# Kernel optimization log

Hardware: AMD Instinct MI355X
Metric: run time of the kernel (lower is better)

## Reference

```python
import jax, jax.numpy as jnp
import numpy as np

N = 50000
E = 800000
F_IN = 500
H = 5          # heads
C = 32         # per-head channels
HID = H * C    # 160
NC = 20        # num_classes
G = 8          # number of graphs in batch
SLOPE_ATT = 0.2   # GATConv attention leaky slope (PyG default)
SLOPE_ACT = 0.01  # F.leaky_relu default


def _layernorm(x, scale, bias, eps=1e-5):
    mu = jnp.mean(x, axis=-1, keepdims=True)
    var = jnp.var(x, axis=-1, keepdims=True)
    return (x - mu) * jax.lax.rsqrt(var + eps) * scale + bias


def _edge_softmax(logits, dst, num_nodes):
    # segment softmax over incoming edges of each destination node
    m = jax.ops.segment_max(logits, dst, num_segments=num_nodes)
    ex = jnp.exp(logits - m[dst])
    s = jax.ops.segment_sum(ex, dst, num_segments=num_nodes)
    return ex / (s[dst] + 1e-16)


def _gat_layer(x, src, dst, W, a_src, a_dst, b):
    n = x.shape[0]
    h = (x @ W).reshape(n, H, C)                       # [N,H,C]
    al_s = jnp.einsum('nhc,hc->nh', h, a_src)          # [N,H]
    al_d = jnp.einsum('nhc,hc->nh', h, a_dst)
    logits = jax.nn.leaky_relu(al_s[src] + al_d[dst], SLOPE_ATT)  # [Et,H]
    alpha = _edge_softmax(logits, dst, n)              # [Et,H]
    msg = h[src] * alpha[..., None]                    # [Et,H,C]
    out = jax.ops.segment_sum(msg, dst, num_segments=n).reshape(n, HID) + b
    return out, alpha


def setup_inputs():
    key = jax.random.key(0)
    ks = jax.random.split(key, 24)
    p = lambda k, shp: jax.random.normal(k, shp, jnp.float32) * 0.05
    x = jax.random.normal(ks[0], (N, F_IN), jnp.float32)
    edge_index = jax.random.randint(ks[1], (2, E), 0, N, jnp.int64)
    batch = jnp.sort(jax.random.randint(ks[2], (N,), 0, G, jnp.int64))
    return {
        'x': x, 'edge_index': edge_index, 'batch': batch,
        'W1': p(ks[3], (F_IN, HID)), 'a_src1': p(ks[4], (H, C)), 'a_dst1': p(ks[5], (H, C)), 'b1': jnp.zeros((HID,), jnp.float32),
        'ln1_s': jnp.ones((HID,), jnp.float32), 'ln1_b': jnp.zeros((HID,), jnp.float32),
        'W2': p(ks[6], (HID, HID)), 'a_src2': p(ks[7], (H, C)), 'a_dst2': p(ks[8], (H, C)), 'b2': jnp.zeros((HID,), jnp.float32),
        'ln2_s': jnp.ones((HID,), jnp.float32), 'ln2_b': jnp.zeros((HID,), jnp.float32),
        'Wm': p(ks[9], (HID, HID)), 'bm': jnp.zeros((HID,), jnp.float32),
        'Wmlp1': p(ks[10], (HID, HID)), 'bmlp1': jnp.zeros((HID,), jnp.float32),
        'ln3_s': jnp.ones((HID,), jnp.float32), 'ln3_b': jnp.zeros((HID,), jnp.float32),
        'Wmlp2': p(ks[11], (HID, NC)), 'bmlp2': jnp.zeros((NC,), jnp.float32),
    }


def reference(x, edge_index, batch, W1, a_src1, a_dst1, b1, ln1_s, ln1_b,
              W2, a_src2, a_dst2, b2, ln2_s, ln2_b, Wm, bm,
              Wmlp1, bmlp1, ln3_s, ln3_b, Wmlp2, bmlp2):
    n = x.shape[0]
    # PyG GATConv adds self-loops by default
    loops = jnp.arange(n, dtype=edge_index.dtype)
    src = jnp.concatenate([edge_index[0], loops])
    dst = jnp.concatenate([edge_index[1], loops])

    h1, alpha1 = _gat_layer(x, src, dst, W1, a_src1, a_dst1, b1)
    h1 = jax.nn.leaky_relu(h1, SLOPE_ACT)
    h1 = _layernorm(h1, ln1_s, ln1_b)      # dropout = identity at eval

    h2, alpha2 = _gat_layer(h1, src, dst, W2, a_src2, a_dst2, b2)
    h2 = jax.nn.leaky_relu(h2, SLOPE_ACT)
    h2 = _layernorm(h2, ln2_s, ln2_b)

    xo = jax.nn.leaky_relu(h2 @ Wm + bm, SLOPE_ACT)   # [N,HID]

    # global_mean_pool over batch assignment
    sums = jax.ops.segment_sum(xo, batch, num_segments=G)
    cnts = jax.ops.segment_sum(jnp.ones((n, 1), xo.dtype), batch, num_segments=G)
    pooled = sums / jnp.maximum(cnts, 1.0)            # [G,HID]

    z = pooled @ Wmlp1 + bmlp1
    z = jax.nn.relu(_layernorm(z, ln3_s, ln3_b))
    rec = z @ Wmlp2 + bmlp2                           # [G,NC]
    return xo, rec, alpha1, alpha2
```

## Files before the change

kernel.cpp:

```cpp
#include <hip/hip_runtime.h>
#include <hip/hip_bf16.h>
#include <cstdint>
#include <cstddef>

#define NN   50000
#define EE   800000
#define ET_  (EE + NN)
#define FIN  500
#define HID_ 160
#define NC_  20
#define GG   8
#define GB1  ((NN + 63) / 64)
#define NK1  16
#define NK2  5

typedef __attribute__((ext_vector_type(8))) short ab8;
typedef __attribute__((ext_vector_type(4))) float f4;

static __device__ __forceinline__ unsigned short f2bf(float v) {
    union { float f; uint32_t u; } c; c.f = v;
    uint32_t r = c.u + 0x7FFFu + ((c.u >> 16) & 1u);
    return (unsigned short)(r >> 16);
}

static __device__ __forceinline__ float2 bf2f2(uint32_t u) {
    union { uint32_t u; float f; } a, b;
    a.u = u << 16;
    b.u = u & 0xffff0000u;
    return make_float2(a.f, b.f);
}

static __device__ __forceinline__ int lbound_i(const int* arr, int n, int val) {
    int lo = 0, hi = n;
    while (lo < hi) { int mid = (lo + hi) >> 1; if (arr[mid] < val) lo = mid + 1; else hi = mid; }
    return lo;
}

__global__ __launch_bounds__(256) void k_hist(const int* __restrict__ ei, int* __restrict__ deg) {
    int e = blockIdx.x * 256 + threadIdx.x;
    if (e >= ET_) return;
    int d = (e < EE) ? ei[EE + e] : (e - EE);
    atomicAdd(&deg[d], 1);
}

__global__ __launch_bounds__(256) void k_scan1(const int* __restrict__ deg, int* __restrict__ rowptr,
                                               int* __restrict__ bsum) {
    __shared__ int s[256];
    int t = threadIdx.x;
    int base = blockIdx.x * 1024 + t * 4;
    int v0 = (base + 0 < NN) ? deg[base + 0] : 0;
    int v1 = (base + 1 < NN) ? deg[base + 1] : 0;
    int v2 = (base + 2 < NN) ? deg[base + 2] : 0;
    int v3 = (base + 3 < NN) ? deg[base + 3] : 0;
    int tot = v0 + v1 + v2 + v3;
    s[t] = tot;
    __syncthreads();
    for (int off = 1; off < 256; off <<= 1) {
        int y = (t >= off) ? s[t - off] : 0;
        __syncthreads();
        s[t] += y;
        __syncthreads();
    }
    int excl = s[t] - tot;
    if (t == 255) bsum[blockIdx.x] = s[255];
    if (base + 0 < NN) rowptr[base + 0] = excl;  excl += v0;
    if (base + 1 < NN) rowptr[base + 1] = excl;  excl += v1;
    if (base + 2 < NN) rowptr[base + 2] = excl;  excl += v2;
    if (base + 3 < NN) rowptr[base + 3] = excl;
}

__global__ void k_scan2(int* __restrict__ bsum, int nb) {
    int t = threadIdx.x;
    int v = (t < nb) ? bsum[t] : 0;
    int orig = v;
    for (int off = 1; off < 64; off <<= 1) {
        int y = __shfl_up(v, off);
        if (t >= off) v += y;
    }
    if (t < nb) bsum[t] = v - orig;
}

__global__ __launch_bounds__(256) void k_scan3(int* __restrict__ rowptr, const int* __restrict__ bsum,
                                               int* __restrict__ cursor) {
    int i = blockIdx.x * 256 + threadIdx.x;
    if (i < NN) {
        int r = rowptr[i] + bsum[i >> 10];
        rowptr[i] = r;
        cursor[i] = r;
    }
    if (i == NN) rowptr[NN] = ET_;
}

__global__ __launch_bounds__(256) void k_scatter(const int* __restrict__ ei, int* __restrict__ cursor,
                                                 int* __restrict__ esrc) {
    int e = blockIdx.x * 256 + threadIdx.x;
    if (e >= ET_) return;
    int s, d;
    if (e < EE) { s = ei[e]; d = ei[EE + e]; } else { s = e - EE; d = e - EE; }
    int slot = atomicAdd(&cursor[d], 1);
    esrc[slot] = s;
}

__global__ __launch_bounds__(256) void k_prep_all(const float* __restrict__ W1, ab8* __restrict__ B1,
                                                  const float* __restrict__ W2, ab8* __restrict__ B2,
                                                  const float* __restrict__ Wm, ab8* __restrict__ Bm,
                                                  float* __restrict__ pooled) {
    int idx = blockIdx.x * 256 + threadIdx.x;
    if (idx < GG * HID_) pooled[idx] = 0.f;
    const int C1 = NK1 * 10 * 64;
    const int C2 = NK2 * 10 * 64;
    const float* W; ab8* Bo; int K, cidx;
    if (idx < C1)                { W = W1; Bo = B1; K = FIN;  cidx = idx; }
    else if (idx < C1 + C2)      { W = W2; Bo = B2; K = HID_; cidx = idx - C1; }
    else if (idx < C1 + 2 * C2)  { W = Wm; Bo = Bm; K = HID_; cidx = idx - C1 - C2; }
    else return;
    int s = cidx / 640, r = cidx % 640;
    int t = r >> 6, l = r & 63;
    int fr = l & 15, q = l >> 4;
    int n  = t * 16 + fr;
    int k0 = s * 32 + q * 8;
    unsigned short pk[8];
#pragma unroll
    for (int j = 0; j < 8; j++) {
        int k = k0 + j;
        pk[j] = (k < K) ? f2bf(W[(size_t)k * HID_ + n]) : (unsigned short)0;
    }
    Bo[cidx] = *reinterpret_cast<ab8*>(pk);
}

__global__ __launch_bounds__(256) void k_conv_x(const float* __restrict__ x, ab8* __restrict__ Apk) {
    int idx = blockIdx.x * 256 + threadIdx.x;
    int tid = idx & 255;
    int s   = (idx >> 8) & (NK1 - 1);
    int blk = idx >> 12;
    int l = tid & 63, w = tid >> 6;
    int fr = l & 15, q = l >> 4;
    int row = blk * 64 + w * 16 + fr;
    int k0 = s * 32 + q * 8;
    unsigned short pk[8] = {0, 0, 0, 0, 0, 0, 0, 0};
    if (row < NN) {
        const float* xr = &x[(size_t)row * FIN];
        if (k0 + 8 <= FIN) {
            const float4* s4 = reinterpret_cast<const float4*>(&xr[k0]);
            float4 u = s4[0], v = s4[1];
            pk[0] = f2bf(u.x); pk[1] = f2bf(u.y); pk[2] = f2bf(u.z); pk[3] = f2bf(u.w);
            pk[4] = f2bf(v.x); pk[5] = f2bf(v.y); pk[6] = f2bf(v.z); pk[7] = f2bf(v.w);
        } else {
#pragma unroll
            for (int j = 0; j < 8; j++)
                if (k0 + j < FIN) pk[j] = f2bf(xr[k0 + j]);
        }
    }
    Apk[idx] = *reinterpret_cast<ab8*>(pk);
}

template<int PKA>
static __device__ __forceinline__ void gemm_body(const void* __restrict__ Av,
                                                 const ab8* __restrict__ Bpk, int nk,
                                                 float* __restrict__ C, __hip_bfloat16* __restrict__ Cb,
                                                 int M, int K,
                                                 const float* __restrict__ bias, int act,
                                                 const float* __restrict__ asrc, const float* __restrict__ adst,
                                                 float* __restrict__ als_o, float* __restrict__ ald_o,
                                                 const int* __restrict__ batch_p, float* __restrict__ pooled) {
    int tid  = threadIdx.x;
    int lane = tid & 63;
    int w    = tid >> 6;
    int fr   = lane & 15;
    int q    = lane >> 4;
    int row0 = blockIdx.x * 64;
    int arow = row0 + w * 16 + fr;
    bool rv  = arow < M;

    f4 acc[10];
#pragma unroll
    for (int t = 0; t < 10; t++) acc[t] = (f4)0.f;

    const ab8* bb  = Bpk + lane;
    const ab8* apk = reinterpret_cast<const ab8*>(Av) + (size_t)blockIdx.x * nk * 256 + tid;
    const unsigned short* Arow = (const unsigned short*)Av;

    auto loadA = [&](int s) -> ab8 {
        if (PKA) return apk[s * 256];
        ab8 a = (ab8)0;
        if (rv) a = *reinterpret_cast<const ab8*>(&Arow[(size_t)arow * K + s * 32 + q * 8]);
        return a;
    };

    ab8 bcur[10], bnx[10];
#pragma unroll
    for (int t = 0; t < 10; t++) bcur[t] = bb[t * 64];
    ab8 a0 = loadA(0);
    ab8 a1 = loadA(1);
    for (int s = 0; s < nk; s++) {
        if (s + 1 < nk) {
#pragma unroll
            for (int t = 0; t < 10; t++) bnx[t] = bb[((s + 1) * 10 + t) * 64];
        }
        ab8 a2 = (ab8)0;
        if (s + 2 < nk) a2 = loadA(s + 2);
#pragma unroll
        for (int t = 0; t < 10; t++)
            acc[t] = __builtin_amdgcn_mfma_f32_16x16x32_bf16(a0, bcur[t], acc[t], 0, 0, 0);
        a0 = a1; a1 = a2;
#pragma unroll
        for (int t = 0; t < 10; t++) bcur[t] = bnx[t];
    }

    if (als_o) {
        float av_s[10], av_d[10];
#pragma unroll
        for (int t = 0; t < 10; t++) { av_s[t] = asrc[t * 16 + fr]; av_d[t] = adst[t * 16 + fr]; }
#pragma unroll
        for (int i = 0; i < 4; i++) {
            int r = row0 + w * 16 + q * 4 + i;
            float ps[5], pd[5];
#pragma unroll
            for (int h = 0; h < 5; h++) {
                ps[h] = acc[2 * h][i] * av_s[2 * h] + acc[2 * h + 1][i] * av_s[2 * h + 1];
                pd[h] = acc[2 * h][i] * av_d[2 * h] + acc[2 * h + 1][i] * av_d[2 * h + 1];
            }
#pragma unroll
            for (int off = 8; off >= 1; off >>= 1)
#pragma unroll
                for (int h = 0; h < 5; h++) {
                    ps[h] += __shfl_xor(ps[h], off);
                    pd[h] += __shfl_xor(pd[h], off);
                }
            if (fr == 0 && r < M) {
#pragma unroll
                for (int h = 0; h < 5; h++) {
                    als_o[(size_t)r * 8 + h] = ps[h];
                    ald_o[(size_t)r * 8 + h] = pd[h];
                }
            }
        }
    }

    int gu = -2;
    if (pooled) {
        int rhi = row0 + 63; if (rhi >= M) rhi = M - 1;
        int gl = batch_p[row0], gh = batch_p[rhi];
        gu = (gl == gh) ? gl : -1;
    }
    float psum[10];
#pragma unroll
    for (int t = 0; t < 10; t++) psum[t] = 0.f;

    int rbase = row0 + w * 16 + q * 4;
#pragma unroll
    for (int t = 0; t < 10; t++) {
        int col = t * 16 + fr;
        float bv = bias ? bias[col] : 0.f;
#pragma unroll
        for (int i = 0; i < 4; i++) {
            int r = rbase + i;
            float v = acc[t][i] + bv;
            if (act) v = v > 0.f ? v : 0.01f * v;
            if (r < M) {
                if (C)  C[(size_t)r * HID_ + col] = v;
                if (Cb) *reinterpret_cast<unsigned short*>(&Cb[(size_t)r * HID_ + col]) = f2bf(v);
                if (gu >= 0) psum[t] += v;
                else if (gu == -1) atomicAdd(&pooled[batch_p[r] * HID_ + col], v);
            }
        }
    }
    if (gu >= 0) {
#pragma unroll
        for (int t = 0; t < 10; t++) {
            psum[t] += __shfl_xor(psum[t], 16);
            psum[t] += __shfl_xor(psum[t], 32);
        }
        if (q == 0) {
#pragma unroll
            for (int t = 0; t < 10; t++)
                atomicAdd(&pooled[gu * HID_ + t * 16 + fr], psum[t]);
        }
    }
}

__global__ __launch_bounds__(256) void k_gemm_pk(const void* __restrict__ Av,
                                                 const ab8* __restrict__ Bpk, int nk,
                                                 float* __restrict__ C, __hip_bfloat16* __restrict__ Cb,
                                                 int M, int K,
                                                 const float* __restrict__ bias, int act,
                                                 const float* __restrict__ asrc, const float* __restrict__ adst,
                                                 float* __restrict__ als_o, float* __restrict__ ald_o,
                                                 const int* __restrict__ batch_p, float* __restrict__ pooled) {
    gemm_body<1>(Av, Bpk, nk, C, Cb, M, K, bias, act, asrc, adst, als_o, ald_o, batch_p, pooled);
}

__global__ __launch_bounds__(256) void k_gemm_rm(const void* __restrict__ Av,
                                                 const ab8* __restrict__ Bpk, int nk,
                                                 float* __restrict__ C, __hip_bfloat16* __restrict__ Cb,
                                                 int M, int K,
                                                 const float* __restrict__ bias, int act,
                                                 const float* __restrict__ asrc, const float* __restrict__ adst,
                                                 float* __restrict__ als_o, float* __restrict__ ald_o,
                                                 const int* __restrict__ batch_p, float* __restrict__ pooled) {
    gemm_body<0>(Av, Bpk, nk, C, Cb, M, K, bias, act, asrc, adst, als_o, ald_o, batch_p, pooled);
}

__global__ __launch_bounds__(256) void k_att_agg(const int* __restrict__ rowptr,
                                                 const int* __restrict__ esrc,
                                                 const float* __restrict__ als, const float* __restrict__ ald,
                                                 const __hip_bfloat16* __restrict__ hmat,
                                                 float* __restrict__ alphap,
                                                 float* __restrict__ invb,
                                                 const float* __restrict__ bias,
                                                 const float* __restrict__ lns, const float* __restrict__ lnb,
                                                 __hip_bfloat16* __restrict__ outb) {
    __shared__ float sExp[4][64 * 5];
    __shared__ int   sSrc[4][64];
    int wv   = threadIdx.x >> 6;
    int lane = threadIdx.x & 63;
    int node = blockIdx.x * 4 + wv;
    if (node >= NN) return;
    int start = rowptr[node], end = rowptr[node + 1];
    int deg = end - start;
    bool fits = (deg <= 64);
    float4 dd4 = *reinterpret_cast<const float4*>(&ald[(size_t)node * 8]);
    float  dd5 = ald[(size_t)node * 8 + 4];
    float ad[5] = {dd4.x, dd4.y, dd4.z, dd4.w, dd5};

    float sm[5] = {0.f, 0.f, 0.f, 0.f, 0.f};
    for (int j = start + lane; j < end; j += 64) {
        int sy = esrc[j];
        int idx = j - start;
        if (fits) sSrc[wv][idx] = sy;
        const float* as = &als[(size_t)sy * 8];
        float4 a4 = *reinterpret_cast<const float4*>(as);
        float  a5 = as[4];
        float asv[5] = {a4.x, a4.y, a4.z, a4.w, a5};
#pragma unroll
        for (int h = 0; h < 5; h++) {
            float l = asv[h] + ad[h];
            l = l > 0.f ? l : 0.2f * l;
            float ex = __expf(fminf(l, 60.f));
            sm[h] += ex;
            if (fits) sExp[wv][idx * 5 + h] = ex;
            else      alphap[(size_t)j * 5 + h] = ex;
        }
    }
#pragma unroll
    for (int off = 32; off >= 1; off >>= 1)
#pragma unroll
        for (int h = 0; h < 5; h++) sm[h] += __shfl_xor(sm[h], off);
    float inv[5];
#pragma unroll
    for (int h = 0; h < 5; h++) inv[h] = 1.f / (sm[h] + 1e-16f);
    if (lane == 0) {
        float* ip = &invb[(size_t)node * 8];
        ip[0] = inv[0]; ip[1] = inv[1]; ip[2] = inv[2]; ip[3] = inv[3]; ip[4] = inv[4];
    }

    int h0 = lane >> 4;
    bool lo16 = lane < 16;
    int c01 = 2 * lane;
    int c2  = 128 + 2 * lane;
    float2 A0 = make_float2(0.f, 0.f), A1 = make_float2(0.f, 0.f);
    float2 A2 = make_float2(0.f, 0.f), A3 = make_float2(0.f, 0.f);
    float2 H0 = make_float2(0.f, 0.f), H1 = make_float2(0.f, 0.f);
    float2 H2 = make_float2(0.f, 0.f), H3 = make_float2(0.f, 0.f);

    if (fits) {
        int idx = 0;
        for (; idx + 3 < deg; idx += 4) {
            int s0 = sSrc[wv][idx], s1 = sSrc[wv][idx + 1];
            int s2 = sSrc[wv][idx + 2], s3 = sSrc[wv][idx + 3];
            float w0 = sExp[wv][(idx + 0) * 5 + h0] * inv[h0];
            float w1 = sExp[wv][(idx + 1) * 5 + h0] * inv[h0];
            float w2 = sExp[wv][(idx + 2) * 5 + h0] * inv[h0];
            float w3 = sExp[wv][(idx + 3) * 5 + h0] * inv[h0];
            const unsigned short* r0 = (const unsigned short*)&hmat[(size_t)s0 * HID_];
            const unsigned short* r1 = (const unsigned short*)&hmat[(size_t)s1 * HID_];
            const unsigned short* r2 = (const unsigned short*)&hmat[(size_t)s2 * HID_];
            const unsigned short* r3 = (const unsigned short*)&hmat[(size_t)s3 * HID_];
            float2 f0 = bf2f2(*reinterpret_cast<const uint32_t*>(&r0[c01]));
            float2 f1 = bf2f2(*reinterpret_cast<const uint32_t*>(&r1[c01]));
            float2 f2 = bf2f2(*reinterpret_cast<const uint32_t*>(&r2[c01]));
            float2 f3 = bf2f2(*reinterpret_cast<const uint32_t*>(&r3[c01]));
            A0.x += w0 * f0.x; A0.y += w0 * f0.y;
            A1.x += w1 * f1.x; A1.y += w1 * f1.y;
            A2.x += w2 * f2.x; A2.y += w2 * f2.y;
            A3.x += w3 * f3.x; A3.y += w3 * f3.y;
            if (lo16) {
                float u0 = sExp[wv][(idx + 0) * 5 + 4] * inv[4];
                float u1 = sExp[wv][(idx + 1) * 5 + 4] * inv[4];
                float u2 = sExp[wv][(idx + 2) * 5 + 4] * inv[4];
                float u3 = sExp[wv][(idx + 3) * 5 + 4] * inv[4];
                float2 g0 = bf2f2(*reinterpret_cast<const uint32_t*>(&r0[c2]));
                float2 g1 = bf2f2(*reinterpret_cast<const uint32_t*>(&r1[c2]));
                float2 g2 = bf2f2(*reinterpret_cast<const uint32_t*>(&r2[c2]));
                float2 g3 = bf2f2(*reinterpret_cast<const uint32_t*>(&r3[c2]));
                H0.x += u0 * g0.x; H0.y += u0 * g0.y;
                H1.x += u1 * g1.x; H1.y += u1 * g1.y;
                H2.x += u2 * g2.x; H2.y += u2 * g2.y;
                H3.x += u3 * g3.x; H3.y += u3 * g3.y;
            }
        }
        for (; idx < deg; idx++) {
            int s0 = sSrc[wv][idx];
            float w0 = sExp[wv][idx * 5 + h0] * inv[h0];
            const unsigned short* r0 = (const unsigned short*)&hmat[(size_t)s0 * HID_];
            float2 f0 = bf2f2(*reinterpret_cast<const uint32_t*>(&r0[c01]));
            A0.x += w0 * f0.x; A0.y += w0 * f0.y;
            if (lo16) {
                float u0 = sExp[wv][idx * 5 + 4] * inv[4];
                float2 g0 = bf2f2(*reinterpret_cast<const uint32_t*>(&r0[c2]));
                H0.x += u0 * g0.x; H0.y += u0 * g0.y;
            }
        }
    } else {
        for (int j = start; j < end; j++) {
            int s0 = esrc[j];
            float w0 = alphap[(size_t)j * 5 + h0] * inv[h0];
            const unsigned short* r0 = (const unsigned short*)&hmat[(size_t)s0 * HID_];
            float2 f0 = bf2f2(*reinterpret_cast<const uint32_t*>(&r0[c01]));
            A0.x += w0 * f0.x; A0.y += w0 * f0.y;
            if (lo16) {
                float u0 = alphap[(size_t)j * 5 + 4] * inv[4];
                float2 g0 = bf2f2(*reinterpret_cast<const uint32_t*>(&r0[c2]));
                H0.x += u0 * g0.x; H0.y += u0 * g0.y;
            }
        }
    }
    float2 A = make_float2(A0.x + A1.x + A2.x + A3.x, A0.y + A1.y + A2.y + A3.y);
    float2 Hh = make_float2(H0.x + H1.x + H2.x + H3.x, H0.y + H1.y + H2.y + H3.y);

    float2 bb = *reinterpret_cast<const float2*>(&bias[c01]);
    float v0 = A.x + bb.x;  v0 = v0 > 0.f ? v0 : 0.01f * v0;
    float v1 = A.y + bb.y;  v1 = v1 > 0.f ? v1 : 0.01f * v1;
    float v2 = 0.f, v3 = 0.f;
    if (lo16) {
        float2 b2 = *reinterpret_cast<const float2*>(&bias[c2]);
        v2 = Hh.x + b2.x; v2 = v2 > 0.f ? v2 : 0.01f * v2;
        v3 = Hh.y + b2.y; v3 = v3 > 0.f ? v3 : 0.01f * v3;
    }
    float s  = v0 + v1 + v2 + v3;
    float sq = v0 * v0 + v1 * v1 + v2 * v2 + v3 * v3;
#pragma unroll
    for (int off = 32; off >= 1; off >>= 1) {
        s  += __shfl_xor(s, off);
        sq += __shfl_xor(sq, off);
    }
    float m = s * (1.f / 160.f);
    float r = rsqrtf(sq * (1.f / 160.f) - m * m + 1e-5f);
    size_t ob = (size_t)node * HID_;
    {
        float2 sc = *reinterpret_cast<const float2*>(&lns[c01]);
        float2 bi = *reinterpret_cast<const float2*>(&lnb[c01]);
        uint32_t pk = (uint32_t)f2bf((v0 - m) * r * sc.x + bi.x)
                    | ((uint32_t)f2bf((v1 - m) * r * sc.y + bi.y) << 16);
        *reinterpret_cast<uint32_t*>(&outb[ob + c01]) = pk;
    }
    if (lo16) {
        float2 sc = *reinterpret_cast<const float2*>(&lns[c2]);
        float2 bi = *reinterpret_cast<const float2*>(&lnb[c2]);
        uint32_t pk = (uint32_t)f2bf((v2 - m) * r * sc.x + bi.x)
                    | ((uint32_t)f2bf((v3 - m) * r * sc.y + bi.y) << 16);
        *reinterpret_cast<uint32_t*>(&outb[ob + c2]) = pk;
    }
}

__global__ __launch_bounds__(256) void k_alpha(const int* __restrict__ ei,
                                               const float* __restrict__ als, const float* __restrict__ ald,
                                               const float* __restrict__ invb,
                                               float* __restrict__ alpha_out) {
    int e = blockIdx.x * 256 + threadIdx.x;
    if (e >= ET_) return;
    int s, d;
    if (e < EE) { s = ei[e]; d = ei[EE + e]; } else { s = e - EE; d = e - EE; }
    const float* as = &als[(size_t)s * 8];
    float4 a4 = *reinterpret_cast<const float4*>(as);
    float  a5 = as[4];
    float asv[5] = {a4.x, a4.y, a4.z, a4.w, a5};
    const float* adp = &ald[(size_t)d * 8];
    float4 d4 = *reinterpret_cast<const float4*>(adp);
    float  d5 = adp[4];
    float adv[5] = {d4.x, d4.y, d4.z, d4.w, d5};
    const float* ip = &invb[(size_t)d * 8];
    float4 i4 = *reinterpret_cast<const float4*>(ip);
    float  i5 = ip[4];
    float ivv[5] = {i4.x, i4.y, i4.z, i4.w, i5};
    float* ao = &alpha_out[(size_t)e * 5];
#pragma unroll
    for (int h = 0; h < 5; h++) {
        float l = asv[h] + adv[h];
        l = l > 0.f ? l : 0.2f * l;
        float ex = __expf(fminf(l, 60.f));
        ao[h] = ex * ivv[h];
    }
}

__global__ __launch_bounds__(256) void k_mlp(const float* __restrict__ pooled, const int* __restrict__ batch,
                                             const float* __restrict__ W1, const float* __restrict__ b1,
                                             const float* __restrict__ lns, const float* __restrict__ lnb,
                                             const float* __restrict__ W2, const float* __restrict__ b2,
                                             float* __restrict__ rec) {
    __shared__ float P[GG][HID_];
    __shared__ float Z[GG][HID_];
    __shared__ float mu[GG], rr[GG], ic[GG];
    int t = threadIdx.x;
    if (t < GG) {
        int lo = lbound_i(batch, NN, t), hi = lbound_i(batch, NN, t + 1);
        ic[t] = 1.f / fmaxf((float)(hi - lo), 1.f);
    }
    __syncthreads();
    for (int i = t; i < GG * HID_; i += 256) P[i / HID_][i % HID_] = pooled[i] * ic[i / HID_];
    __syncthreads();
    for (int i = t; i < GG * HID_; i += 256) {
        int g = i / HID_, j = i % HID_;
        float acc = b1[j];
        for (int k = 0; k < HID_; k++) acc += P[g][k] * W1[k * HID_ + j];
        Z[g][j] = acc;
    }
    __syncthreads();
    if (t < GG) {
        float s = 0.f, sq = 0.f;
        for (int k = 0; k < HID_; k++) { float z = Z[t][k]; s += z; sq += z * z; }
        float m = s / (float)HID_;
        mu[t] = m;
        rr[t] = rsqrtf(sq / (float)HID_ - m * m + 1e-5f);
    }
    __syncthreads();
    for (int i = t; i < GG * HID_; i += 256) {
        int g = i / HID_, j = i % HID_;
        float z = (Z[g][j] - mu[g]) * rr[g] * lns[j] + lnb[j];
        Z[g][j] = fmaxf(z, 0.f);
    }
    __syncthreads();
    for (int i = t; i < GG * NC_; i += 256) {
        int g = i / NC_, j = i % NC_;
        float acc = b2[j];
        for (int k = 0; k < HID_; k++) acc += Z[g][k] * W2[k * NC_ + j];
        rec[g * NC_ + j] = acc;
    }
}

extern "C" void kernel_launch(void* const* d_in, const int* in_sizes, int n_in,
                              void* d_out, int out_size, void* d_ws, size_t ws_size,
                              hipStream_t stream) {
    const float* x    = (const float*)d_in[0];
    const int*   ei   = (const int*)d_in[1];
    const int*   batch= (const int*)d_in[2];
    const float* W1   = (const float*)d_in[3];
    const float* as1  = (const float*)d_in[4];
    const float* ad1  = (const float*)d_in[5];
    const float* b1   = (const float*)d_in[6];
    const float* ln1s = (const float*)d_in[7];
    const float* ln1b = (const float*)d_in[8];
    const float* W2   = (const float*)d_in[9];
    const float* as2  = (const float*)d_in[10];
    const float* ad2  = (const float*)d_in[11];
    const float* b2   = (const float*)d_in[12];
    const float* ln2s = (const float*)d_in[13];
    const float* ln2b = (const float*)d_in[14];
    const float* Wm   = (const float*)d_in[15];
    const float* bm   = (const float*)d_in[16];
    const float* Wm1  = (const float*)d_in[17];
    const float* bm1  = (const float*)d_in[18];
    const float* ln3s = (const float*)d_in[19];
    const float* ln3b = (const float*)d_in[20];
    const float* Wm2  = (const float*)d_in[21];
    const float* bm2  = (const float*)d_in[22];

    float* out    = (float*)d_out;
    float* xo     = out;
    float* rec    = out + (size_t)NN * HID_;
    float* alpha1 = rec + GG * NC_;
    float* alpha2 = alpha1 + (size_t)ET_ * 5;

    char* w = (char*)d_ws;
    auto carve = [&](size_t bytes) { char* p = w; w += (bytes + 255) & ~(size_t)255; return p; };
    int*   deg    = (int*)carve((size_t)NN * 4);
    int*   rowptr = (int*)carve((size_t)(NN + 1) * 4);
    int*   cursor = (int*)carve((size_t)NN * 4);
    int*   esrc   = (int*)carve((size_t)ET_ * 4);
    int*   bsum   = (int*)carve(64 * 4);
    __hip_bfloat16* hbuf  = (__hip_bfloat16*)carve((size_t)NN * HID_ * 2);
    __hip_bfloat16* xbufb = (__hip_bfloat16*)carve((size_t)NN * HID_ * 2);
    float* alphap = (float*)carve((size_t)ET_ * 5 * 4);
    float* als    = (float*)carve((size_t)NN * 8 * 4);
    float* ald    = (float*)carve((size_t)NN * 8 * 4);
    float* invb   = (float*)carve((size_t)NN * 8 * 4);
    float* pooled = (float*)carve((size_t)GG * HID_ * 4);
    ab8*   B1pk   = (ab8*)carve((size_t)NK1 * 10 * 64 * 16);
    ab8*   B2pk   = (ab8*)carve((size_t)NK2 * 10 * 64 * 16);
    ab8*   Bmpk   = (ab8*)carve((size_t)NK2 * 10 * 64 * 16);
    ab8*   Apk    = (ab8*)d_out;

    hipMemsetAsync(deg, 0, (size_t)NN * 4, stream);
    k_hist<<<(ET_ + 255) / 256, 256, 0, stream>>>(ei, deg);
    int nb = (NN + 1023) / 1024;
    k_scan1<<<nb, 256, 0, stream>>>(deg, rowptr, bsum);
    k_scan2<<<1, 64, 0, stream>>>(bsum, nb);
    k_scan3<<<(NN + 1 + 255) / 256, 256, 0, stream>>>(rowptr, bsum, cursor);
    k_scatter<<<(ET_ + 255) / 256, 256, 0, stream>>>(ei, cursor, esrc);

    const int PREP = NK1 * 10 * 64 + 2 * NK2 * 10 * 64;
    k_prep_all<<<(PREP + 255) / 256, 256, 0, stream>>>(W1, B1pk, W2, B2pk, Wm, Bmpk, pooled);
    k_conv_x<<<GB1 * NK1, 256, 0, stream>>>(x, Apk);

    const int NWB = (NN + 3) / 4;
    const int EB  = (ET_ + 255) / 256;

    k_gemm_pk<<<GB1, 256, 0, stream>>>(Apk, B1pk, NK1, nullptr, hbuf, NN, FIN, nullptr, 0,
                                       as1, ad1, als, ald, nullptr, nullptr);
    k_att_agg<<<NWB, 256, 0, stream>>>(rowptr, esrc, als, ald, hbuf, alphap, invb,
                                       b1, ln1s, ln1b, xbufb);
    k_alpha<<<EB, 256, 0, stream>>>(ei, als, ald, invb, alpha1);

    k_gemm_rm<<<GB1, 256, 0, stream>>>(xbufb, B2pk, NK2, nullptr, hbuf, NN, HID_, nullptr, 0,
                                       as2, ad2, als, ald, nullptr, nullptr);
    k_att_agg<<<NWB, 256, 0, stream>>>(rowptr, esrc, als, ald, hbuf, alphap, invb,
                                       b2, ln2s, ln2b, xbufb);
    k_alpha<<<EB, 256, 0, stream>>>(ei, als, ald, invb, alpha2);

    k_gemm_rm<<<GB1, 256, 0, stream>>>(xbufb, Bmpk, NK2, xo, nullptr, NN, HID_, bm, 1,
                                       nullptr, nullptr, nullptr, nullptr, batch, pooled);
    k_mlp<<<1, 256, 0, stream>>>(pooled, batch, Wm1, bm1, ln3s, ln3b, Wm2, bm2, rec);
}
```

Before: 630.6 us.

## Write aggregation output directly in MFMA-packed layout for downstream GEMMs

The attention-aggregation kernel now shuffles its bf16 LayerNorm outputs across lanes and stores them as 16-byte chunks in the fragment-packed A layout the GEMM consumes, so layers 2 and 3 use the packed-load GEMM path instead of strided row-major loads with bounds checks. The softmax normalisation is also folded into the shared-memory exp weights once per edge instead of multiplying by the inverse sum in the inner gather loop. The cost is extra cross-lane shuffles and a more complex store index in the aggregation epilogue.

```diff
diff --git a/kernel.cpp b/kernel.cpp
--- a/kernel.cpp
+++ b/kernel.cpp
@@ -154,11 +154,10 @@
     Apk[idx] = *reinterpret_cast<ab8*>(pk);
 }
 
-template<int PKA>
-static __device__ __forceinline__ void gemm_body(const void* __restrict__ Av,
+static __device__ __forceinline__ void gemm_body(const ab8* __restrict__ Apk,
                                                  const ab8* __restrict__ Bpk, int nk,
                                                  float* __restrict__ C, __hip_bfloat16* __restrict__ Cb,
-                                                 int M, int K,
+                                                 int M,
                                                  const float* __restrict__ bias, int act,
                                                  const float* __restrict__ asrc, const float* __restrict__ adst,
                                                  float* __restrict__ als_o, float* __restrict__ ald_o,
@@ -169,36 +168,26 @@
     int fr   = lane & 15;
     int q    = lane >> 4;
     int row0 = blockIdx.x * 64;
-    int arow = row0 + w * 16 + fr;
-    bool rv  = arow < M;
 
     f4 acc[10];
 #pragma unroll
     for (int t = 0; t < 10; t++) acc[t] = (f4)0.f;
 
     const ab8* bb  = Bpk + lane;
-    const ab8* apk = reinterpret_cast<const ab8*>(Av) + (size_t)blockIdx.x * nk * 256 + tid;
-    const unsigned short* Arow = (const unsigned short*)Av;
-
-    auto loadA = [&](int s) -> ab8 {
-        if (PKA) return apk[s * 256];
-        ab8 a = (ab8)0;
-        if (rv) a = *reinterpret_cast<const ab8*>(&Arow[(size_t)arow * K + s * 32 + q * 8]);
-        return a;
-    };
+    const ab8* apk = Apk + (size_t)blockIdx.x * nk * 256 + tid;
 
     ab8 bcur[10], bnx[10];
 #pragma unroll
     for (int t = 0; t < 10; t++) bcur[t] = bb[t * 64];
-    ab8 a0 = loadA(0);
-    ab8 a1 = loadA(1);
+    ab8 a0 = apk[0];
+    ab8 a1 = apk[256];
     for (int s = 0; s < nk; s++) {
         if (s + 1 < nk) {
 #pragma unroll
             for (int t = 0; t < 10; t++) bnx[t] = bb[((s + 1) * 10 + t) * 64];
         }
         ab8 a2 = (ab8)0;
-        if (s + 2 < nk) a2 = loadA(s + 2);
+        if (s + 2 < nk) a2 = apk[(s + 2) * 256];
 #pragma unroll
         for (int t = 0; t < 10; t++)
             acc[t] = __builtin_amdgcn_mfma_f32_16x16x32_bf16(a0, bcur[t], acc[t], 0, 0, 0);
@@ -279,26 +268,15 @@
     }
 }
 
-__global__ __launch_bounds__(256) void k_gemm_pk(const void* __restrict__ Av,
+__global__ __launch_bounds__(256) void k_gemm_pk(const ab8* __restrict__ Apk,
                                                  const ab8* __restrict__ Bpk, int nk,
                                                  float* __restrict__ C, __hip_bfloat16* __restrict__ Cb,
-                                                 int M, int K,
+                                                 int M,
                                                  const float* __restrict__ bias, int act,
                                                  const float* __restrict__ asrc, const float* __restrict__ adst,
                                                  float* __restrict__ als_o, float* __restrict__ ald_o,
                                                  const int* __restrict__ batch_p, float* __restrict__ pooled) {
-    gemm_body<1>(Av, Bpk, nk, C, Cb, M, K, bias, act, asrc, adst, als_o, ald_o, batch_p, pooled);
-}
-
-__global__ __launch_bounds__(256) void k_gemm_rm(const void* __restrict__ Av,
-                                                 const ab8* __restrict__ Bpk, int nk,
-                                                 float* __restrict__ C, __hip_bfloat16* __restrict__ Cb,
-                                                 int M, int K,
-                                                 const float* __restrict__ bias, int act,
-                                                 const float* __restrict__ asrc, const float* __restrict__ adst,
-                                                 float* __restrict__ als_o, float* __restrict__ ald_o,
-                                                 const int* __restrict__ batch_p, float* __restrict__ pooled) {
-    gemm_body<0>(Av, Bpk, nk, C, Cb, M, K, bias, act, asrc, adst, als_o, ald_o, batch_p, pooled);
+    gemm_body(Apk, Bpk, nk, C, Cb, M, bias, act, asrc, adst, als_o, ald_o, batch_p, pooled);
 }
 
 __global__ __launch_bounds__(256) void k_att_agg(const int* __restrict__ rowptr,
@@ -309,7 +287,7 @@
                                                  float* __restrict__ invb,
                                                  const float* __restrict__ bias,
                                                  const float* __restrict__ lns, const float* __restrict__ lnb,
-                                                 __hip_bfloat16* __restrict__ outb) {
+                                                 uint4* __restrict__ xpk) {
     __shared__ float sExp[4][64 * 5];
     __shared__ int   sSrc[4][64];
     int wv   = threadIdx.x >> 6;
@@ -353,6 +331,10 @@
         float* ip = &invb[(size_t)node * 8];
         ip[0] = inv[0]; ip[1] = inv[1]; ip[2] = inv[2]; ip[3] = inv[3]; ip[4] = inv[4];
     }
+    if (fits && lane < deg) {
+#pragma unroll
+        for (int h = 0; h < 5; h++) sExp[wv][lane * 5 + h] *= inv[h];
+    }
 
     int h0 = lane >> 4;
     bool lo16 = lane < 16;
@@ -368,10 +350,10 @@
         for (; idx + 3 < deg; idx += 4) {
             int s0 = sSrc[wv][idx], s1 = sSrc[wv][idx + 1];
             int s2 = sSrc[wv][idx + 2], s3 = sSrc[wv][idx + 3];
-            float w0 = sExp[wv][(idx + 0) * 5 + h0] * inv[h0];
-            float w1 = sExp[wv][(idx + 1) * 5 + h0] * inv[h0];
-            float w2 = sExp[wv][(idx + 2) * 5 + h0] * inv[h0];
-            float w3 = sExp[wv][(idx + 3) * 5 + h0] * inv[h0];
+            float w0 = sExp[wv][(idx + 0) * 5 + h0];
+            float w1 = sExp[wv][(idx + 1) * 5 + h0];
+            float w2 = sExp[wv][(idx + 2) * 5 + h0];
+            float w3 = sExp[wv][(idx + 3) * 5 + h0];
             const unsigned short* r0 = (const unsigned short*)&hmat[(size_t)s0 * HID_];
             const unsigned short* r1 = (const unsigned short*)&hmat[(size_t)s1 * HID_];
             const unsigned short* r2 = (const unsigned short*)&hmat[(size_t)s2 * HID_];
@@ -385,10 +367,10 @@
             A2.x += w2 * f2.x; A2.y += w2 * f2.y;
             A3.x += w3 * f3.x; A3.y += w3 * f3.y;
             if (lo16) {
-                float u0 = sExp[wv][(idx + 0) * 5 + 4] * inv[4];
-                float u1 = sExp[wv][(idx + 1) * 5 + 4] * inv[4];
-                float u2 = sExp[wv][(idx + 2) * 5 + 4] * inv[4];
-                float u3 = sExp[wv][(idx + 3) * 5 + 4] * inv[4];
+                float u0 = sExp[wv][(idx + 0) * 5 + 4];
+                float u1 = sExp[wv][(idx + 1) * 5 + 4];
+                float u2 = sExp[wv][(idx + 2) * 5 + 4];
+                float u3 = sExp[wv][(idx + 3) * 5 + 4];
                 float2 g0 = bf2f2(*reinterpret_cast<const uint32_t*>(&r0[c2]));
                 float2 g1 = bf2f2(*reinterpret_cast<const uint32_t*>(&r1[c2]));
                 float2 g2 = bf2f2(*reinterpret_cast<const uint32_t*>(&r2[c2]));
@@ -401,12 +383,12 @@
         }
         for (; idx < deg; idx++) {
             int s0 = sSrc[wv][idx];
-            float w0 = sExp[wv][idx * 5 + h0] * inv[h0];
+            float w0 = sExp[wv][idx * 5 + h0];
             const unsigned short* r0 = (const unsigned short*)&hmat[(size_t)s0 * HID_];
             float2 f0 = bf2f2(*reinterpret_cast<const uint32_t*>(&r0[c01]));
             A0.x += w0 * f0.x; A0.y += w0 * f0.y;
             if (lo16) {
-                float u0 = sExp[wv][idx * 5 + 4] * inv[4];
+                float u0 = sExp[wv][idx * 5 + 4];
                 float2 g0 = bf2f2(*reinterpret_cast<const uint32_t*>(&r0[c2]));
                 H0.x += u0 * g0.x; H0.y += u0 * g0.y;
             }
@@ -446,20 +428,35 @@
     }
     float m = s * (1.f / 160.f);
     float r = rsqrtf(sq * (1.f / 160.f) - m * m + 1e-5f);
-    size_t ob = (size_t)node * HID_;
+    uint32_t pk1, pk2 = 0u;
     {
         float2 sc = *reinterpret_cast<const float2*>(&lns[c01]);
         float2 bi = *reinterpret_cast<const float2*>(&lnb[c01]);
-        uint32_t pk = (uint32_t)f2bf((v0 - m) * r * sc.x + bi.x)
-                    | ((uint32_t)f2bf((v1 - m) * r * sc.y + bi.y) << 16);
-        *reinterpret_cast<uint32_t*>(&outb[ob + c01]) = pk;
+        pk1 = (uint32_t)f2bf((v0 - m) * r * sc.x + bi.x)
+            | ((uint32_t)f2bf((v1 - m) * r * sc.y + bi.y) << 16);
     }
     if (lo16) {
         float2 sc = *reinterpret_cast<const float2*>(&lns[c2]);
         float2 bi = *reinterpret_cast<const float2*>(&lnb[c2]);
-        uint32_t pk = (uint32_t)f2bf((v2 - m) * r * sc.x + bi.x)
-                    | ((uint32_t)f2bf((v3 - m) * r * sc.y + bi.y) << 16);
-        *reinterpret_cast<uint32_t*>(&outb[ob + c2]) = pk;
+        pk2 = (uint32_t)f2bf((v2 - m) * r * sc.x + bi.x)
+            | ((uint32_t)f2bf((v3 - m) * r * sc.y + bi.y) << 16);
+    }
+    int j = lane;
+    int srcb = (j < 16) ? (4 * j) : (4 * ((j - 16) & 15));
+    uint32_t a0w = __shfl(pk1, srcb + 0), a1w = __shfl(pk1, srcb + 1);
+    uint32_t a2w = __shfl(pk1, srcb + 2), a3w = __shfl(pk1, srcb + 3);
+    uint32_t b0w = __shfl(pk2, srcb + 0), b1w = __shfl(pk2, srcb + 1);
+    uint32_t b2w = __shfl(pk2, srcb + 2), b3w = __shfl(pk2, srcb + 3);
+    if (j < 20) {
+        uint4 val;
+        val.x = (j < 16) ? a0w : b0w;
+        val.y = (j < 16) ? a1w : b1w;
+        val.z = (j < 16) ? a2w : b2w;
+        val.w = (j < 16) ? a3w : b3w;
+        int blk = node >> 6, wq = (node >> 4) & 3, fr = node & 15;
+        int ks = j >> 2, q = j & 3;
+        size_t cidx = (size_t)(blk * NK2 + ks) * 256 + wq * 64 + q * 16 + fr;
+        xpk[cidx] = val;
     }
 }
 
@@ -578,8 +575,8 @@
     int*   cursor = (int*)carve((size_t)NN * 4);
     int*   esrc   = (int*)carve((size_t)ET_ * 4);
     int*   bsum   = (int*)carve(64 * 4);
-    __hip_bfloat16* hbuf  = (__hip_bfloat16*)carve((size_t)NN * HID_ * 2);
-    __hip_bfloat16* xbufb = (__hip_bfloat16*)carve((size_t)NN * HID_ * 2);
+    __hip_bfloat16* hbuf = (__hip_bfloat16*)carve((size_t)NN * HID_ * 2);
+    uint4* xpk    = (uint4*)carve((size_t)GB1 * NK2 * 256 * 16);
     float* alphap = (float*)carve((size_t)ET_ * 5 * 4);
     float* als    = (float*)carve((size_t)NN * 8 * 4);
     float* ald    = (float*)carve((size_t)NN * 8 * 4);
@@ -605,19 +602,19 @@
     const int NWB = (NN + 3) / 4;
     const int EB  = (ET_ + 255) / 256;
 
-    k_gemm_pk<<<GB1, 256, 0, stream>>>(Apk, B1pk, NK1, nullptr, hbuf, NN, FIN, nullptr, 0,
+    k_gemm_pk<<<GB1, 256, 0, stream>>>(Apk, B1pk, NK1, nullptr, hbuf, NN, nullptr, 0,
                                        as1, ad1, als, ald, nullptr, nullptr);
     k_att_agg<<<NWB, 256, 0, stream>>>(rowptr, esrc, als, ald, hbuf, alphap, invb,
-                                       b1, ln1s, ln1b, xbufb);
+                                       b1, ln1s, ln1b, xpk);
     k_alpha<<<EB, 256, 0, stream>>>(ei, als, ald, invb, alpha1);
 
-    k_gemm_rm<<<GB1, 256, 0, stream>>>(xbufb, B2pk, NK2, nullptr, hbuf, NN, HID_, nullptr, 0,
+    k_gemm_pk<<<GB1, 256, 0, stream>>>((const ab8*)xpk, B2pk, NK2, nullptr, hbuf, NN, nullptr, 0,
                                        as2, ad2, als, ald, nullptr, nullptr);
     k_att_agg<<<NWB, 256, 0, stream>>>(rowptr, esrc, als, ald, hbuf, alphap, invb,
-                                       b2, ln2s, ln2b, xbufb);
+                                       b2, ln2s, ln2b, xpk);
     k_alpha<<<EB, 256, 0, stream>>>(ei, als, ald, invb, alpha2);
 
-    k_gemm_rm<<<GB1, 256, 0, stream>>>(xbufb, Bmpk, NK2, xo, nullptr, NN, HID_, bm, 1,
+    k_gemm_pk<<<GB1, 256, 0, stream>>>((const ab8*)xpk, Bmpk, NK2, xo, nullptr, NN, bm, 1,
                                        nullptr, nullptr, nullptr, nullptr, batch, pooled);
     k_mlp<<<1, 256, 0, stream>>>(pooled, batch, Wm1, bm1, ln3s, ln3b, Wm2, bm2, rec);
 }
```

Measured after the change: 643.2 us. No clear change (+2.0%).
